# Kernel optimization log

Hardware: AMD Instinct MI355X
Metric: run time of the kernel (lower is better)

The kernel has to match this reference:

```python
import jax, jax.numpy as jnp
import numpy as np

N_NODES = 100000
N_EDGES = 800000
D = 128
N_HEADS = 8
D_HEAD = D // N_HEADS


def setup_inputs() -> dict:
    key = jax.random.key(0)
    ks = jax.random.split(key, 8)
    x = jax.random.normal(ks[0], (N_NODES, D), dtype=jnp.float32)
    src = jax.random.randint(ks[1], (N_EDGES,), 0, N_NODES, dtype=jnp.int32)
    dst = jax.random.randint(ks[2], (N_EDGES,), 0, N_NODES, dtype=jnp.int32)
    s = 1.0 / np.sqrt(D)
    # torch nn.Linear convention: y = x @ W.T + b, W ~ U(-1/sqrt(fan_in), ...)
    W_qkv = jax.random.uniform(ks[3], (3 * D, D), jnp.float32, -s, s)
    b_qkv = jax.random.uniform(ks[4], (3 * D,), jnp.float32, -s, s)
    W_out = jax.random.uniform(ks[5], (D, D), jnp.float32, -s, s)
    b_out = jax.random.uniform(ks[6], (D,), jnp.float32, -s, s)
    return {"x": x, "W_qkv": W_qkv, "b_qkv": b_qkv, "W_out": W_out,
            "b_out": b_out, "src": src, "dst": dst}


def reference(x, W_qkv, b_qkv, W_out, b_out, src, dst):
    N = x.shape[0]
    coef = D_HEAD ** -0.5
    qkv = (x @ W_qkv.T + b_qkv).reshape(N, N_HEADS, 3 * D_HEAD)
    q = qkv[..., :D_HEAD]          # [N, H, dh]
    k = qkv[..., D_HEAD:2 * D_HEAD]
    v = qkv[..., 2 * D_HEAD:]
    # u_dot_v: per-edge dot of source k and destination q -> [E, H]
    scores = jnp.einsum('ehd,ehd->eh', k[src], q[dst]) * coef
    # edge_softmax: softmax over edges grouped by destination node
    m = jax.ops.segment_max(scores, dst, num_segments=N)
    m = jnp.where(jnp.isfinite(m), m, 0.0)  # guard zero in-degree nodes
    p = jnp.exp(scores - m[dst])
    denom = jax.ops.segment_sum(p, dst, num_segments=N)
    probs = p / denom[dst]                   # [E, H]
    # u_mul_e_sum: weighted aggregation of source v into destination
    out = jax.ops.segment_sum(v[src] * probs[:, :, None], dst, num_segments=N)
    out = out.reshape(N, D)
    return out @ W_out.T + b_out
```

## Files before the change

kernel.cpp:

```cpp
#include <hip/hip_runtime.h>
#include <hip/hip_bf16.h>

#define N_NODES 100000
#define N_EDGES 800000
#define NB1 98

typedef __attribute__((ext_vector_type(8))) short short8;
typedef __attribute__((ext_vector_type(4))) float f32x4;

__device__ __forceinline__ float bf2f(ushort u) {
    union { unsigned i; float f; } x; x.i = ((unsigned)u) << 16; return x.f;
}
__device__ __forceinline__ ushort f2bf(float f) {
    union { float f; unsigned u; } x { f };
    unsigned r = x.u + 0x7FFF + ((x.u >> 16) & 1);
    return (ushort)(r >> 16);
}

__global__ __launch_bounds__(256) void cvt_bf16(
    const float* __restrict__ in, ushort* __restrict__ out, int n4)
{
    int i = blockIdx.x * 256 + threadIdx.x;
    if (i >= n4) return;
    float4 v = reinterpret_cast<const float4*>(in)[i];
    ushort4 o;
    o.x = f2bf(v.x); o.y = f2bf(v.y); o.z = f2bf(v.z); o.w = f2bf(v.w);
    reinterpret_cast<ushort4*>(out)[i] = o;
}

__global__ __launch_bounds__(128) void permute_w(
    const float* __restrict__ Wq, const float* __restrict__ bq,
    ushort* __restrict__ Wqb, float* __restrict__ bqp)
{
    int j = blockIdx.x;
    int h = j / 48, r = j % 48;
    int p = (r < 16) ? h * 16 + r
          : (r < 32) ? 128 + h * 16 + (r - 16)
                     : 256 + h * 16 + (r - 32);
    const float* row = Wq + (size_t)j * 128;
    ushort* orow = Wqb + (size_t)p * 128;
    orow[threadIdx.x] = f2bf(row[threadIdx.x]);
    if (threadIdx.x == 0) bqp[p] = bq[j];
}

template<int A_F32, int OUT_BF16>
__global__ __launch_bounds__(256) void gemm_mfma(
    const void* __restrict__ Av, const ushort* __restrict__ B,
    const float* __restrict__ bias, void* __restrict__ Cv,
    int M, int ldc)
{
    __shared__ ushort As[128][72];
    __shared__ ushort Bs[128][72];
    const int t = threadIdx.x;
    const int lane = t & 63;
    const int w = t >> 6;
    const int wm = w >> 1, wn = w & 1;
    const int n0 = blockIdx.x * 128;
    const int j0 = blockIdx.y * 128;

    f32x4 acc[4][4];
    #pragma unroll
    for (int i = 0; i < 4; ++i)
        #pragma unroll
        for (int j = 0; j < 4; ++j) acc[i][j] = (f32x4){0.f, 0.f, 0.f, 0.f};

    for (int kb = 0; kb < 128; kb += 64) {
        #pragma unroll
        for (int it = 0; it < 4; ++it) {
            int c = it * 256 + t;
            int row = c >> 3, g = c & 7;
            int ar = n0 + row; if (ar >= M) ar = M - 1;
            if (A_F32) {
                const float* ap = (const float*)Av + (size_t)ar * 128 + kb + g * 8;
                float4 a0 = *reinterpret_cast<const float4*>(ap);
                float4 a1 = *reinterpret_cast<const float4*>(ap + 4);
                short8 o;
                o[0] = (short)f2bf(a0.x); o[1] = (short)f2bf(a0.y);
                o[2] = (short)f2bf(a0.z); o[3] = (short)f2bf(a0.w);
                o[4] = (short)f2bf(a1.x); o[5] = (short)f2bf(a1.y);
                o[6] = (short)f2bf(a1.z); o[7] = (short)f2bf(a1.w);
                *reinterpret_cast<short8*>(&As[row][g * 8]) = o;
            } else {
                *reinterpret_cast<short8*>(&As[row][g * 8]) =
                    *reinterpret_cast<const short8*>(
                        (const ushort*)Av + (size_t)ar * 128 + kb + g * 8);
            }
            *reinterpret_cast<short8*>(&Bs[row][g * 8]) =
                *reinterpret_cast<const short8*>(B + (size_t)(j0 + row) * 128 + kb + g * 8);
        }
        __syncthreads();
        #pragma unroll
        for (int kf = 0; kf < 2; ++kf) {
            short8 af[4], bfr[4];
            #pragma unroll
            for (int mf = 0; mf < 4; ++mf)
                af[mf] = *reinterpret_cast<const short8*>(
                    &As[wm * 64 + mf * 16 + (lane & 15)][kf * 32 + (lane >> 4) * 8]);
            #pragma unroll
            for (int nf = 0; nf < 4; ++nf)
                bfr[nf] = *reinterpret_cast<const short8*>(
                    &Bs[wn * 64 + nf * 16 + (lane & 15)][kf * 32 + (lane >> 4) * 8]);
            #pragma unroll
            for (int mf = 0; mf < 4; ++mf)
                #pragma unroll
                for (int nf = 0; nf < 4; ++nf)
                    acc[mf][nf] = __builtin_amdgcn_mfma_f32_16x16x32_bf16(
                        af[mf], bfr[nf], acc[mf][nf], 0, 0, 0);
        }
        __syncthreads();
    }

    const int r0 = (lane >> 4) * 4, cc = lane & 15;
    #pragma unroll
    for (int mf = 0; mf < 4; ++mf) {
        #pragma unroll
        for (int j = 0; j < 4; ++j) {
            int row = n0 + wm * 64 + mf * 16 + r0 + j;
            if (row >= M) continue;
            #pragma unroll
            for (int nf = 0; nf < 4; ++nf) {
                int col = j0 + wn * 64 + nf * 16 + cc;
                float v = acc[mf][nf][j] + bias[col];
                if (OUT_BF16)
                    ((ushort*)Cv)[(size_t)row * ldc + col] = f2bf(v);
                else
                    ((float*)Cv)[(size_t)row * ldc + col] = v;
            }
        }
    }
}

__global__ __launch_bounds__(256) void count_dst(
    const int* __restrict__ dst, int* __restrict__ counts)
{
    int e = blockIdx.x * 256 + threadIdx.x;
    if (e < N_EDGES) atomicAdd(&counts[dst[e]], 1);
}

__global__ __launch_bounds__(1024) void scan1(
    const int* __restrict__ counts, int* __restrict__ row_start,
    int* __restrict__ bsums)
{
    __shared__ int sd[1024];
    int t = threadIdx.x, i = blockIdx.x * 1024 + t;
    int v = (i < N_NODES) ? counts[i] : 0;
    sd[t] = v; __syncthreads();
    for (int off = 1; off < 1024; off <<= 1) {
        int x = (t >= off) ? sd[t - off] : 0;
        __syncthreads();
        sd[t] += x;
        __syncthreads();
    }
    if (i < N_NODES) row_start[i] = sd[t] - v;
    if (t == 1023) bsums[blockIdx.x] = sd[1023];
}

__global__ __launch_bounds__(128) void scan2(
    const int* __restrict__ bsums, int* __restrict__ boffs)
{
    __shared__ int sd[128];
    int t = threadIdx.x;
    int v = (t < NB1) ? bsums[t] : 0;
    sd[t] = v; __syncthreads();
    for (int off = 1; off < 128; off <<= 1) {
        int x = (t >= off) ? sd[t - off] : 0;
        __syncthreads();
        sd[t] += x;
        __syncthreads();
    }
    if (t < NB1) boffs[t] = sd[t] - v;
}

__global__ __launch_bounds__(256) void scan3(
    int* __restrict__ row_start, const int* __restrict__ boffs)
{
    int i = blockIdx.x * 256 + threadIdx.x;
    if (i < N_NODES) row_start[i] += boffs[i >> 10];
    if (i == 0) row_start[N_NODES] = N_EDGES;
}

__global__ __launch_bounds__(256) void fill_csr(
    const int* __restrict__ src, const int* __restrict__ dst,
    const int* __restrict__ row_start, int* __restrict__ fillc,
    int* __restrict__ csr_src)
{
    int e = blockIdx.x * 256 + threadIdx.x;
    if (e >= N_EDGES) return;
    int d = dst[e];
    int pos = row_start[d] + atomicAdd(&fillc[d], 1);
    csr_src[pos] = src[e];
}

__global__ __launch_bounds__(256) void fused_attn(
    const ushort* __restrict__ qkvp, const int* __restrict__ row_start,
    const int* __restrict__ csr_src, ushort* __restrict__ attnb)
{
    int node = (blockIdx.x * 256 + threadIdx.x) >> 6;
    if (node >= N_NODES) return;
    int lane = threadIdx.x & 63;

    unsigned qb = *reinterpret_cast<const unsigned*>(
        qkvp + (size_t)node * 384 + lane * 2);
    float q0 = bf2f((ushort)qb), q1 = bf2f((ushort)(qb >> 16));

    int beg = row_start[node], end = row_start[node + 1];
    float denom = 0.f, a0 = 0.f, a1 = 0.f;

#define GATHER(s, kk, vv) { \
        const ushort* rp = qkvp + (size_t)(s) * 384 + 128 + lane * 2; \
        kk = *reinterpret_cast<const unsigned*>(rp); \
        vv = *reinterpret_cast<const unsigned*>(rp + 128); }
#define EDGE(kk, vv) { \
        float ps = bf2f((ushort)(kk)) * q0 + bf2f((ushort)((kk) >> 16)) * q1; \
        ps += __shfl_xor(ps, 1); \
        ps += __shfl_xor(ps, 2); \
        ps += __shfl_xor(ps, 4); \
        float p = __expf(ps * 0.25f); \
        denom += p; \
        a0 += p * bf2f((ushort)(vv)); \
        a1 += p * bf2f((ushort)((vv) >> 16)); }

    int i = beg;
    for (; i + 4 <= end; i += 4) {
        int s0 = csr_src[i], s1 = csr_src[i + 1];
        int s2 = csr_src[i + 2], s3 = csr_src[i + 3];
        unsigned k0, v0, k1, v1, k2, v2, k3, v3;
        GATHER(s0, k0, v0); GATHER(s1, k1, v1);
        GATHER(s2, k2, v2); GATHER(s3, k3, v3);
        EDGE(k0, v0); EDGE(k1, v1); EDGE(k2, v2); EDGE(k3, v3);
    }
    for (; i < end; ++i) {
        int s = csr_src[i];
        unsigned kk, vv;
        GATHER(s, kk, vv);
        EDGE(kk, vv);
    }
#undef GATHER
#undef EDGE

    float inv = (end > beg) ? 1.f / denom : 0.f;
    unsigned o = ((unsigned)f2bf(a1 * inv) << 16) | (unsigned)f2bf(a0 * inv);
    *reinterpret_cast<unsigned*>(attnb + (size_t)node * 128 + lane * 2) = o;
}

extern "C" void kernel_launch(void* const* d_in, const int* in_sizes, int n_in,
                              void* d_out, int out_size, void* d_ws, size_t ws_size,
                              hipStream_t stream) {
    const float* x     = (const float*)d_in[0];
    const float* W_qkv = (const float*)d_in[1];
    const float* b_qkv = (const float*)d_in[2];
    const float* W_out = (const float*)d_in[3];
    const float* b_out = (const float*)d_in[4];
    const int*   src   = (const int*)d_in[5];
    const int*   dst   = (const int*)d_in[6];
    float* out = (float*)d_out;

    char* w = (char*)d_ws;
    ushort* qkvp     = (ushort*)(w);
    ushort* attnb    = (ushort*)(w + 76800000);
    ushort* Wqb      = (ushort*)(w + 102400000);
    ushort* Wob      = (ushort*)(w + 102498304);
    float*  bqp      = (float*)(w + 102531072);
    int*    counts   = (int*)(w + 102532608);
    int*    fillc    = (int*)(w + 102932608);
    int*    row_start= (int*)(w + 103332608);
    int*    bsums    = (int*)(w + 103732736);
    int*    boffs    = (int*)(w + 103733248);
    int*    csr_src  = (int*)(w + 103733760);

    hipMemsetAsync(counts, 0, 800000, stream);

    permute_w<<<384, 128, 0, stream>>>(W_qkv, b_qkv, Wqb, bqp);
    cvt_bf16<<<16, 256, 0, stream>>>(W_out, Wob, 4096);

    gemm_mfma<1, 1><<<dim3(782, 3), 256, 0, stream>>>(
        (const void*)x, Wqb, bqp, (void*)qkvp, N_NODES, 384);

    count_dst<<<3125, 256, 0, stream>>>(dst, counts);
    scan1<<<NB1, 1024, 0, stream>>>(counts, row_start, bsums);
    scan2<<<1, 128, 0, stream>>>(bsums, boffs);
    scan3<<<391, 256, 0, stream>>>(row_start, boffs);
    fill_csr<<<3125, 256, 0, stream>>>(src, dst, row_start, fillc, csr_src);

    fused_attn<<<25000, 256, 0, stream>>>(qkvp, row_start, csr_src, attnb);

    gemm_mfma<0, 0><<<dim3(782, 1), 256, 0, stream>>>(
        (const void*)attnb, Wob, b_out, (void*)out, N_NODES, 128);
}
```

Baseline: 312.7 us.

## Fuse CSR build into cooperative kernel, interleave K/V layout, vectorize GEMM stores

The five CSR-construction kernels (count, three scan stages, fill) become one cooperative kernel that uses grid-wide syncs, cutting launch overhead. The two weight-prep kernels are merged into one. The QKV weight permutation now interleaves K and V per lane so each edge gather in the attention kernel is a single 8-byte load, and the edge loop is unrolled to 8 to keep more gathers in flight. The GEMM swaps the MFMA operands so each lane holds 4 consecutive output columns, which allows vectorized stores. Grid-wide syncs add their own latency, and the wider unroll raises register pressure.

New measurement: 505.2 us. +61.6%, slower.

```diff
diff --git a/kernel.cpp b/kernel.cpp
--- a/kernel.cpp
+++ b/kernel.cpp
@@ -1,12 +1,16 @@
 #include <hip/hip_runtime.h>
 #include <hip/hip_bf16.h>
+#include <hip/hip_cooperative_groups.h>
+
+namespace cg = cooperative_groups;
 
 #define N_NODES 100000
 #define N_EDGES 800000
-#define NB1 98
+#define CSR_BLOCKS 391
 
 typedef __attribute__((ext_vector_type(8))) short short8;
 typedef __attribute__((ext_vector_type(4))) float f32x4;
+typedef __attribute__((ext_vector_type(2))) unsigned int u32x2;
 
 __device__ __forceinline__ float bf2f(ushort u) {
     union { unsigned i; float f; } x; x.i = ((unsigned)u) << 16; return x.f;
@@ -17,30 +21,23 @@
     return (ushort)(r >> 16);
 }
 
-__global__ __launch_bounds__(256) void cvt_bf16(
-    const float* __restrict__ in, ushort* __restrict__ out, int n4)
-{
-    int i = blockIdx.x * 256 + threadIdx.x;
-    if (i >= n4) return;
-    float4 v = reinterpret_cast<const float4*>(in)[i];
-    ushort4 o;
-    o.x = f2bf(v.x); o.y = f2bf(v.y); o.z = f2bf(v.z); o.w = f2bf(v.w);
-    reinterpret_cast<ushort4*>(out)[i] = o;
-}
-
-__global__ __launch_bounds__(128) void permute_w(
+__global__ __launch_bounds__(128) void prep_weights(
     const float* __restrict__ Wq, const float* __restrict__ bq,
-    ushort* __restrict__ Wqb, float* __restrict__ bqp)
+    const float* __restrict__ Wo,
+    ushort* __restrict__ Wqb, float* __restrict__ bqp, ushort* __restrict__ Wob)
 {
     int j = blockIdx.x;
-    int h = j / 48, r = j % 48;
-    int p = (r < 16) ? h * 16 + r
-          : (r < 32) ? 128 + h * 16 + (r - 16)
-                     : 256 + h * 16 + (r - 32);
-    const float* row = Wq + (size_t)j * 128;
-    ushort* orow = Wqb + (size_t)p * 128;
-    orow[threadIdx.x] = f2bf(row[threadIdx.x]);
-    if (threadIdx.x == 0) bqp[p] = bq[j];
+    if (j < 384) {
+        int h = j / 48, r = j % 48, p;
+        if (r < 16)      p = h * 16 + r;
+        else if (r < 32) { int d = r - 16; p = 128 + (h * 8 + (d >> 1)) * 4 + (d & 1); }
+        else             { int d = r - 32; p = 128 + (h * 8 + (d >> 1)) * 4 + 2 + (d & 1); }
+        Wqb[(size_t)p * 128 + threadIdx.x] = f2bf(Wq[(size_t)j * 128 + threadIdx.x]);
+        if (threadIdx.x == 0) bqp[p] = bq[j];
+    } else {
+        int j2 = j - 384;
+        Wob[(size_t)j2 * 128 + threadIdx.x] = f2bf(Wo[(size_t)j2 * 128 + threadIdx.x]);
+    }
 }
 
 template<int A_F32, int OUT_BF16>
@@ -105,90 +102,90 @@
                 #pragma unroll
                 for (int nf = 0; nf < 4; ++nf)
                     acc[mf][nf] = __builtin_amdgcn_mfma_f32_16x16x32_bf16(
-                        af[mf], bfr[nf], acc[mf][nf], 0, 0, 0);
-        }
-        __syncthreads();
-    }
-
-    const int r0 = (lane >> 4) * 4, cc = lane & 15;
+                        bfr[nf], af[mf], acc[mf][nf], 0, 0, 0);
+        }
+        __syncthreads();
+    }
+
+    const int r = lane & 15, c4 = (lane >> 4) * 4;
     #pragma unroll
     for (int mf = 0; mf < 4; ++mf) {
-        #pragma unroll
-        for (int j = 0; j < 4; ++j) {
-            int row = n0 + wm * 64 + mf * 16 + r0 + j;
-            if (row >= M) continue;
-            #pragma unroll
-            for (int nf = 0; nf < 4; ++nf) {
-                int col = j0 + wn * 64 + nf * 16 + cc;
-                float v = acc[mf][nf][j] + bias[col];
-                if (OUT_BF16)
-                    ((ushort*)Cv)[(size_t)row * ldc + col] = f2bf(v);
-                else
-                    ((float*)Cv)[(size_t)row * ldc + col] = v;
+        int row = n0 + wm * 64 + mf * 16 + r;
+        if (row >= M) continue;
+        #pragma unroll
+        for (int nf = 0; nf < 4; ++nf) {
+            int col = j0 + wn * 64 + nf * 16 + c4;
+            f32x4 a = acc[mf][nf];
+            float v0 = a[0] + bias[col],     v1 = a[1] + bias[col + 1];
+            float v2 = a[2] + bias[col + 2], v3 = a[3] + bias[col + 3];
+            if (OUT_BF16) {
+                u32x2 u;
+                u[0] = (unsigned)f2bf(v0) | ((unsigned)f2bf(v1) << 16);
+                u[1] = (unsigned)f2bf(v2) | ((unsigned)f2bf(v3) << 16);
+                *reinterpret_cast<u32x2*>((ushort*)Cv + (size_t)row * ldc + col) = u;
+            } else {
+                float4 o = {v0, v1, v2, v3};
+                *reinterpret_cast<float4*>((float*)Cv + (size_t)row * ldc + col) = o;
             }
         }
     }
 }
 
-__global__ __launch_bounds__(256) void count_dst(
-    const int* __restrict__ dst, int* __restrict__ counts)
-{
-    int e = blockIdx.x * 256 + threadIdx.x;
-    if (e < N_EDGES) atomicAdd(&counts[dst[e]], 1);
-}
-
-__global__ __launch_bounds__(1024) void scan1(
-    const int* __restrict__ counts, int* __restrict__ row_start,
-    int* __restrict__ bsums)
-{
-    __shared__ int sd[1024];
-    int t = threadIdx.x, i = blockIdx.x * 1024 + t;
-    int v = (i < N_NODES) ? counts[i] : 0;
+__global__ __launch_bounds__(256) void build_csr(
+    const int* __restrict__ src, const int* __restrict__ dst,
+    int* __restrict__ counts, int* __restrict__ fillc,
+    int* __restrict__ row_start, int* __restrict__ bsums,
+    int* __restrict__ boffs, int* __restrict__ csr_src)
+{
+    cg::grid_group grid = cg::this_grid();
+    const int t = threadIdx.x, b = blockIdx.x;
+    const int gid = b * 256 + t;
+    const int gsz = CSR_BLOCKS * 256;
+
+    for (int e = gid; e < N_EDGES; e += gsz)
+        atomicAdd(&counts[dst[e]], 1);
+    grid.sync();
+
+    __shared__ int sd[256];
+    int v = (gid < N_NODES) ? counts[gid] : 0;
     sd[t] = v; __syncthreads();
-    for (int off = 1; off < 1024; off <<= 1) {
+    #pragma unroll
+    for (int off = 1; off < 256; off <<= 1) {
         int x = (t >= off) ? sd[t - off] : 0;
         __syncthreads();
         sd[t] += x;
         __syncthreads();
     }
-    if (i < N_NODES) row_start[i] = sd[t] - v;
-    if (t == 1023) bsums[blockIdx.x] = sd[1023];
-}
-
-__global__ __launch_bounds__(128) void scan2(
-    const int* __restrict__ bsums, int* __restrict__ boffs)
-{
-    __shared__ int sd[128];
-    int t = threadIdx.x;
-    int v = (t < NB1) ? bsums[t] : 0;
-    sd[t] = v; __syncthreads();
-    for (int off = 1; off < 128; off <<= 1) {
-        int x = (t >= off) ? sd[t - off] : 0;
-        __syncthreads();
-        sd[t] += x;
-        __syncthreads();
-    }
-    if (t < NB1) boffs[t] = sd[t] - v;
-}
-
-__global__ __launch_bounds__(256) void scan3(
-    int* __restrict__ row_start, const int* __restrict__ boffs)
-{
-    int i = blockIdx.x * 256 + threadIdx.x;
-    if (i < N_NODES) row_start[i] += boffs[i >> 10];
-    if (i == 0) row_start[N_NODES] = N_EDGES;
-}
-
-__global__ __launch_bounds__(256) void fill_csr(
-    const int* __restrict__ src, const int* __restrict__ dst,
-    const int* __restrict__ row_start, int* __restrict__ fillc,
-    int* __restrict__ csr_src)
-{
-    int e = blockIdx.x * 256 + threadIdx.x;
-    if (e >= N_EDGES) return;
-    int d = dst[e];
-    int pos = row_start[d] + atomicAdd(&fillc[d], 1);
-    csr_src[pos] = src[e];
+    if (gid < N_NODES) row_start[gid] = sd[t] - v;
+    if (t == 255) bsums[b] = sd[255];
+    grid.sync();
+
+    if (b == 0 && t < 64) {
+        int carry = 0;
+        for (int c = 0; c < CSR_BLOCKS; c += 64) {
+            int idx = c + t;
+            int orig = (idx < CSR_BLOCKS) ? bsums[idx] : 0;
+            int val = orig;
+            #pragma unroll
+            for (int off = 1; off < 64; off <<= 1) {
+                int y = __shfl_up(val, off);
+                if (t >= off) val += y;
+            }
+            if (idx < CSR_BLOCKS) boffs[idx] = carry + val - orig;
+            carry += __shfl(val, 63);
+        }
+    }
+    grid.sync();
+
+    if (gid < N_NODES) row_start[gid] += boffs[b];
+    if (gid == 0) row_start[N_NODES] = N_EDGES;
+    grid.sync();
+
+    for (int e = gid; e < N_EDGES; e += gsz) {
+        int d = dst[e];
+        int pos = row_start[d] + atomicAdd(&fillc[d], 1);
+        csr_src[pos] = src[e];
+    }
 }
 
 __global__ __launch_bounds__(256) void fused_attn(
@@ -205,35 +202,36 @@
 
     int beg = row_start[node], end = row_start[node + 1];
     float denom = 0.f, a0 = 0.f, a1 = 0.f;
-
-#define GATHER(s, kk, vv) { \
-        const ushort* rp = qkvp + (size_t)(s) * 384 + 128 + lane * 2; \
-        kk = *reinterpret_cast<const unsigned*>(rp); \
-        vv = *reinterpret_cast<const unsigned*>(rp + 128); }
-#define EDGE(kk, vv) { \
-        float ps = bf2f((ushort)(kk)) * q0 + bf2f((ushort)((kk) >> 16)) * q1; \
+    const ushort* kvbase = qkvp + 128 + lane * 4;
+
+#define GATHER(s, u) u = *reinterpret_cast<const u32x2*>(kvbase + (size_t)(s) * 384);
+#define EDGE(u) { \
+        float ps = bf2f((ushort)u[0]) * q0 + bf2f((ushort)(u[0] >> 16)) * q1; \
         ps += __shfl_xor(ps, 1); \
         ps += __shfl_xor(ps, 2); \
         ps += __shfl_xor(ps, 4); \
         float p = __expf(ps * 0.25f); \
         denom += p; \
-        a0 += p * bf2f((ushort)(vv)); \
-        a1 += p * bf2f((ushort)((vv) >> 16)); }
+        a0 += p * bf2f((ushort)u[1]); \
+        a1 += p * bf2f((ushort)(u[1] >> 16)); }
 
     int i = beg;
-    for (; i + 4 <= end; i += 4) {
-        int s0 = csr_src[i], s1 = csr_src[i + 1];
+    for (; i + 8 <= end; i += 8) {
+        int s0 = csr_src[i],     s1 = csr_src[i + 1];
         int s2 = csr_src[i + 2], s3 = csr_src[i + 3];
-        unsigned k0, v0, k1, v1, k2, v2, k3, v3;
-        GATHER(s0, k0, v0); GATHER(s1, k1, v1);
-        GATHER(s2, k2, v2); GATHER(s3, k3, v3);
-        EDGE(k0, v0); EDGE(k1, v1); EDGE(k2, v2); EDGE(k3, v3);
+        int s4 = csr_src[i + 4], s5 = csr_src[i + 5];
+        int s6 = csr_src[i + 6], s7 = csr_src[i + 7];
+        u32x2 u0, u1, u2, u3, u4, u5, u6, u7;
+        GATHER(s0, u0); GATHER(s1, u1); GATHER(s2, u2); GATHER(s3, u3);
+        GATHER(s4, u4); GATHER(s5, u5); GATHER(s6, u6); GATHER(s7, u7);
+        EDGE(u0); EDGE(u1); EDGE(u2); EDGE(u3);
+        EDGE(u4); EDGE(u5); EDGE(u6); EDGE(u7);
     }
     for (; i < end; ++i) {
         int s = csr_src[i];
-        unsigned kk, vv;
-        GATHER(s, kk, vv);
-        EDGE(kk, vv);
+        u32x2 u;
+        GATHER(s, u);
+        EDGE(u);
     }
 #undef GATHER
 #undef EDGE
@@ -264,23 +262,24 @@
     int*    counts   = (int*)(w + 102532608);
     int*    fillc    = (int*)(w + 102932608);
     int*    row_start= (int*)(w + 103332608);
-    int*    bsums    = (int*)(w + 103732736);
-    int*    boffs    = (int*)(w + 103733248);
-    int*    csr_src  = (int*)(w + 103733760);
+    int*    bsums    = (int*)(w + 103732624);
+    int*    boffs    = (int*)(w + 103734224);
+    int*    csr_src  = (int*)(w + 103735824);
 
     hipMemsetAsync(counts, 0, 800000, stream);
 
-    permute_w<<<384, 128, 0, stream>>>(W_qkv, b_qkv, Wqb, bqp);
-    cvt_bf16<<<16, 256, 0, stream>>>(W_out, Wob, 4096);
+    prep_weights<<<512, 128, 0, stream>>>(W_qkv, b_qkv, W_out, Wqb, bqp, Wob);
 
     gemm_mfma<1, 1><<<dim3(782, 3), 256, 0, stream>>>(
         (const void*)x, Wqb, bqp, (void*)qkvp, N_NODES, 384);
 
-    count_dst<<<3125, 256, 0, stream>>>(dst, counts);
-    scan1<<<NB1, 1024, 0, stream>>>(counts, row_start, bsums);
-    scan2<<<1, 128, 0, stream>>>(bsums, boffs);
-    scan3<<<391, 256, 0, stream>>>(row_start, boffs);
-    fill_csr<<<3125, 256, 0, stream>>>(src, dst, row_start, fillc, csr_src);
+    {
+        void* args[] = {(void*)&src, (void*)&dst, (void*)&counts, (void*)&fillc,
+                        (void*)&row_start, (void*)&bsums, (void*)&boffs,
+                        (void*)&csr_src};
+        hipLaunchCooperativeKernel((const void*)build_csr, dim3(CSR_BLOCKS),
+                                   dim3(256), args, 0, stream);
+    }
 
     fused_attn<<<25000, 256, 0, stream>>>(qkvp, row_start, csr_src, attnb);
 
```
